# Kernel tuning notes

Measured on AMD Instinct MI355X. Metric: run time of the kernel, lower is better.

Reference implementation:

```python
import jax, jax.numpy as jnp
import numpy as np

# dims
B, L, V, E, H = 8, 2048, 32000, 512, 512
NUM_LAYERS, D_STATE, EXPAND, HEADDIM, D_CONV = 4, 64, 2, 64, 4
D_INNER = EXPAND * H                      # 1024
N_HEADS = D_INNER // HEADDIM              # 16
CONV_DIM = D_INNER + 2 * D_STATE          # 1152
D_PROJ = 2 * D_INNER + 2 * D_STATE + N_HEADS  # 2192 (z, xBC, dt)
PAD_IDX = 0
EPS = 1e-5


def silu(x):
    return x * jax.nn.sigmoid(x)


def _flip_len(x, lengths):
    # length-aware flip: reverse only the first `length` positions per sample
    t = jnp.arange(x.shape[1])[None, :]                 # (1, L)
    Lm = lengths[:, None]                               # (B, 1)
    idx = jnp.where(t < Lm, Lm - 1 - t, t)              # (B, L)
    return jnp.take_along_axis(x, idx[:, :, None], axis=1)


def _mamba2(x, W_in, conv_w, conv_b, dt_bias, A_log, Dp, norm_w, W_out):
    # Mamba2 forward (mamba_ssm semantics): in_proj -> causal depthwise conv ->
    # selective scan (SSD recurrence) -> gated RMSNorm -> out_proj.
    b, l, _ = x.shape
    zxbcdt = x @ W_in.T                                  # (b, l, D_PROJ)
    z, xBC, dt = jnp.split(zxbcdt, [D_INNER, D_INNER + CONV_DIM], axis=-1)
    # causal depthwise conv over time, kernel D_CONV
    xBC = jnp.transpose(xBC, (0, 2, 1))                  # (b, CONV_DIM, l)
    xBC = jax.lax.conv_general_dilated(
        xBC, conv_w[:, None, :], (1,), [(D_CONV - 1, 0)],
        feature_group_count=CONV_DIM)
    xBC = silu(xBC + conv_b[None, :, None])
    xBC = jnp.transpose(xBC, (0, 2, 1))                  # (b, l, CONV_DIM)
    xh, Bm, Cm = jnp.split(xBC, [D_INNER, D_INNER + D_STATE], axis=-1)
    dt = jax.nn.softplus(dt + dt_bias)                   # (b, l, nh)
    dA = jnp.exp(dt * (-jnp.exp(A_log)))                 # (b, l, nh)
    xh = xh.reshape(b, l, N_HEADS, HEADDIM)

    def step(s, inp):
        x_t, B_t, C_t, dA_t, dt_t = inp
        # s: (b, nh, hd, ds)
        s = s * dA_t[:, :, None, None] + (dt_t[:, :, None] * x_t)[..., None] * B_t[:, None, None, :]
        y = jnp.einsum('bnps,bs->bnp', s, C_t) + Dp[None, :, None] * x_t
        return s, y

    xs = (xh.transpose(1, 0, 2, 3), Bm.transpose(1, 0, 2), Cm.transpose(1, 0, 2),
          dA.transpose(1, 0, 2), dt.transpose(1, 0, 2))
    s0 = jnp.zeros((b, N_HEADS, HEADDIM, D_STATE), x.dtype)
    _, ys = jax.lax.scan(step, s0, xs)
    y = ys.transpose(1, 0, 2, 3).reshape(b, l, D_INNER)
    # gated RMSNorm then out projection
    y = y * silu(z)
    y = y * jax.lax.rsqrt(jnp.mean(y * y, axis=-1, keepdims=True) + EPS) * norm_w
    return y @ W_out.T


def _layernorm(x, g, b):
    mu = jnp.mean(x, axis=-1, keepdims=True)
    xc = x - mu
    var = jnp.mean(xc * xc, axis=-1, keepdims=True)
    return xc * jax.lax.rsqrt(var + EPS) * g + b


def setup_inputs() -> dict:
    key = jax.random.key(0)
    ks = iter(jax.random.split(key, 32))
    def nrm(shape, scale=0.02):
        return jax.random.normal(next(ks), shape, jnp.float32) * scale
    input_tokens = jax.random.randint(next(ks), (B, L), 1, V)
    src_lengths = jax.random.randint(next(ks), (B,), L // 2, L + 1)
    emb = nrm((V, E)).at[PAD_IDX].set(0.0)
    W_inp, b_inp = nrm((H, E)), jnp.zeros((H,), jnp.float32)
    m_Win = nrm((NUM_LAYERS, 2, D_PROJ, H))
    m_convw = nrm((NUM_LAYERS, 2, CONV_DIM, D_CONV), 0.2)
    m_convb = jnp.zeros((NUM_LAYERS, 2, CONV_DIM), jnp.float32)
    m_dtb = nrm((NUM_LAYERS, 2, N_HEADS), 0.5)
    m_Alog = jnp.log(jax.random.uniform(next(ks), (NUM_LAYERS, 2, N_HEADS), minval=1.0, maxval=16.0))
    m_D = jnp.ones((NUM_LAYERS, 2, N_HEADS), jnp.float32)
    m_norm = jnp.ones((NUM_LAYERS, 2, D_INNER), jnp.float32)
    m_Wout = nrm((NUM_LAYERS, 2, H, D_INNER))
    blk_Wo = nrm((NUM_LAYERS, H, 2 * H))
    blk_bo = jnp.zeros((NUM_LAYERS, H), jnp.float32)
    ln_g = jnp.ones((NUM_LAYERS, H), jnp.float32)
    ln_b = jnp.zeros((NUM_LAYERS, H), jnp.float32)
    W_enc, b_enc = nrm((2 * H, H)), jnp.zeros((2 * H,), jnp.float32)
    W_ad, b_ad = nrm((H, 2 * H)), jnp.zeros((H,), jnp.float32)
    return dict(input_tokens=input_tokens, src_lengths=src_lengths, emb=emb,
                W_inp=W_inp, b_inp=b_inp, m_Win=m_Win, m_convw=m_convw,
                m_convb=m_convb, m_dtb=m_dtb, m_Alog=m_Alog, m_D=m_D,
                m_norm=m_norm, m_Wout=m_Wout, blk_Wo=blk_Wo, blk_bo=blk_bo,
                ln_g=ln_g, ln_b=ln_b, W_enc=W_enc, b_enc=b_enc, W_ad=W_ad, b_ad=b_ad)


def reference(input_tokens, src_lengths, emb, W_inp, b_inp, m_Win, m_convw,
              m_convb, m_dtb, m_Alog, m_D, m_norm, m_Wout, blk_Wo, blk_bo,
              ln_g, ln_b, W_enc, b_enc, W_ad, b_ad):
    h = emb[input_tokens] @ W_inp.T + b_inp              # (B, L, H)
    for i in range(NUM_LAYERS):
        fwd = _mamba2(h, m_Win[i, 0], m_convw[i, 0], m_convb[i, 0], m_dtb[i, 0],
                      m_Alog[i, 0], m_D[i, 0], m_norm[i, 0], m_Wout[i, 0])
        hf = _flip_len(h, src_lengths)
        bwd = _mamba2(hf, m_Win[i, 1], m_convw[i, 1], m_convb[i, 1], m_dtb[i, 1],
                      m_Alog[i, 1], m_D[i, 1], m_norm[i, 1], m_Wout[i, 1])
        bwd = _flip_len(bwd, src_lengths)
        comb = jnp.concatenate([fwd, bwd], axis=-1)      # (B, L, 2H)
        out = comb @ blk_Wo[i].T + blk_bo[i]
        h = _layernorm(out + h, ln_g[i], ln_b[i])
    encoder_outputs = h @ W_enc.T + b_enc                # (B, L, 2H)
    mask = (jnp.arange(L)[None, :] < src_lengths[:, None]).astype(h.dtype)[..., None]
    denom = jnp.clip(src_lengths.astype(h.dtype), 1.0)[:, None]
    pooled = jnp.sum(encoder_outputs * mask, axis=1) / denom
    encoder_hidden = jnp.tanh(pooled @ W_ad.T + b_ad)[None]   # (1, B, H)
    return encoder_outputs, encoder_hidden
```

## Files before the change

### kernel.cpp

```cpp
#include <hip/hip_runtime.h>
#include <hip/hip_bf16.h>
#include <math.h>

using bf16 = __hip_bfloat16;
typedef __bf16 bf16x8 __attribute__((ext_vector_type(8)));
typedef float f32x4 __attribute__((ext_vector_type(4)));

#define B2F(x) __bfloat162float(x)
#define F2B(x) __float2bfloat16(x)

__device__ inline short f2bs(float x) { bf16 b = F2B(x); return *(short*)&b; }
__device__ inline float bs2f(short x) { bf16 b; *(short*)&b = x; return B2F(b); }

static constexpr int D_PROJ = 2192, CONV_DIM = 1152;
static constexpr int NCHUNK = 8, CLEN = 256;

static constexpr size_t OFF_H    = 0;
static constexpr size_t OFF_ZX   = 16777216;
static constexpr size_t OFF_XC   = 88604672;
static constexpr size_t OFF_S    = 126353408;
static constexpr size_t OFF_PT   = 143130624;
static constexpr size_t OFF_PC   = 144179200;
static constexpr size_t OFF_DTV  = 144183296;
static constexpr size_t OFF_DAV  = 145231872;
static constexpr size_t OFF_GIDX = 146280448;
static constexpr size_t OFF_POOL = 146345984;
static constexpr size_t OFF_WBF   = 146378752;
static constexpr size_t WBF_WIN   = 0;
static constexpr size_t WBF_WOUT  = 17956864;
static constexpr size_t WBF_BLK   = 26345472;
static constexpr size_t WBF_ENC   = 30539776;
static constexpr size_t WBF_BYTES = 31588352;

__global__ void k_wcvt(const float* __restrict__ src, bf16* __restrict__ dst, long n8)
{
    long i = (long)blockIdx.x * 256 + threadIdx.x;
    if (i >= n8) return;
    const float4* s = (const float4*)(src + i * 8);
    float4 f0 = s[0], f1 = s[1];
    short o[8];
    o[0] = f2bs(f0.x); o[1] = f2bs(f0.y); o[2] = f2bs(f0.z); o[3] = f2bs(f0.w);
    o[4] = f2bs(f1.x); o[5] = f2bs(f1.y); o[6] = f2bs(f1.z); o[7] = f2bs(f1.w);
    *(int4*)&dst[i * 8] = *(int4*)o;
}

__device__ inline void gl_lds16(const void* g, void* l)
{
    __builtin_amdgcn_global_load_lds(
        (const __attribute__((address_space(1))) unsigned int*)g,
        (__attribute__((address_space(3))) unsigned int*)l,
        16, 0, 0);
}

template<bool CF32>
__global__ __launch_bounds__(256, 2)
void k_gemm_bf(const bf16* __restrict__ A, const int* __restrict__ gatherIdx,
               const bf16* __restrict__ Wb, const float* __restrict__ bias,
               void* __restrict__ Cp, int M, int N, int K, int ldc, int coff)
{
    __shared__ union UU {
        struct { __align__(16) short As[128 * 64]; __align__(16) short Bs[128 * 64]; } ab;
        __align__(16) short Cs2[128 * 136];
        __align__(16) float Cs4[CF32 ? 128 * 132 : 4];
    } u;

    const int tid  = threadIdx.x;
    const int m0   = blockIdx.y * 128;
    const int n0   = blockIdx.x * 128;
    const int wave = tid >> 6, lane = tid & 63;
    const int l15  = lane & 15, quad = lane >> 4;
    const int wm   = (wave & 1) * 64, wn = (wave >> 1) * 64;

    const int sr   = lane >> 3;
    const int slot = lane & 7;
    const bf16* asrc[4];
    const bf16* bsrc[4];
    int ldsoff[4];
#pragma unroll
    for (int t = 0; t < 4; ++t) {
        int row = wave * 32 + t * 8 + sr;
        long arow = m0 + row;
        if (gatherIdx) arow = gatherIdx[m0 + row];
        int sl = ((slot ^ (row & 7)) * 8);
        asrc[t] = A + arow * (long)K + sl;
        int wr = n0 + row; if (wr > N - 1) wr = N - 1;
        bsrc[t] = Wb + (long)wr * K + sl;
        ldsoff[t] = (wave * 32 + t * 8) * 64;
    }

    int aoff[2][4], boff[2][4];
#pragma unroll
    for (int ks = 0; ks < 2; ++ks) {
        int swz = (((ks << 2) | quad) ^ (l15 & 7)) * 8;
#pragma unroll
        for (int i = 0; i < 4; ++i) {
            aoff[ks][i] = (wm + i * 16 + l15) * 64 + swz;
            boff[ks][i] = (wn + i * 16 + l15) * 64 + swz;
        }
    }

    f32x4 acc[4][4];
#pragma unroll
    for (int i = 0; i < 4; ++i)
#pragma unroll
        for (int j = 0; j < 4; ++j) acc[i][j] = f32x4{0.f, 0.f, 0.f, 0.f};

    for (int k0 = 0; k0 < K; k0 += 64) {
#pragma unroll
        for (int t = 0; t < 4; ++t) gl_lds16(asrc[t] + k0, &u.ab.As[ldsoff[t]]);
#pragma unroll
        for (int t = 0; t < 4; ++t) gl_lds16(bsrc[t] + k0, &u.ab.Bs[ldsoff[t]]);
        __syncthreads();

        bf16x8 af[2][4], bfr[2][4];
#pragma unroll
        for (int ks = 0; ks < 2; ++ks)
#pragma unroll
            for (int i = 0; i < 4; ++i) {
                af[ks][i]  = *(const bf16x8*)&u.ab.As[aoff[ks][i]];
                bfr[ks][i] = *(const bf16x8*)&u.ab.Bs[boff[ks][i]];
            }
#pragma unroll
        for (int ks = 0; ks < 2; ++ks)
#pragma unroll
            for (int i = 0; i < 4; ++i)
#pragma unroll
                for (int j = 0; j < 4; ++j)
                    acc[i][j] = __builtin_amdgcn_mfma_f32_16x16x32_bf16(af[ks][i], bfr[ks][j], acc[i][j], 0, 0, 0);
        __syncthreads();
    }

    __syncthreads();
    if (!CF32) {
#pragma unroll
        for (int j = 0; j < 4; ++j) {
            int lcol = wn + j * 16 + l15;
            int gcol = n0 + lcol;
            float bvv = (bias && gcol < N) ? bias[gcol] : 0.f;
#pragma unroll
            for (int i = 0; i < 4; ++i)
#pragma unroll
                for (int r = 0; r < 4; ++r)
                    u.Cs2[(wm + i * 16 + quad * 4 + r) * 136 + lcol] = f2bs(acc[i][j][r] + bvv);
        }
        __syncthreads();
        for (int i2 = tid; i2 < 2048; i2 += 256) {
            int lrow = i2 >> 4, seg = i2 & 15;
            int col0 = n0 + seg * 8;
            if (col0 < N) {
                int4 v = *(int4*)&u.Cs2[lrow * 136 + seg * 8];
                *(int4*)&((bf16*)Cp)[(long)(m0 + lrow) * ldc + coff + col0] = v;
            }
        }
    } else {
#pragma unroll
        for (int j = 0; j < 4; ++j) {
            int lcol = wn + j * 16 + l15;
            int gcol = n0 + lcol;
            float bvv = (bias && gcol < N) ? bias[gcol] : 0.f;
#pragma unroll
            for (int i = 0; i < 4; ++i)
#pragma unroll
                for (int r = 0; r < 4; ++r)
                    u.Cs4[(wm + i * 16 + quad * 4 + r) * 132 + lcol] = acc[i][j][r] + bvv;
        }
        __syncthreads();
        for (int i2 = tid; i2 < 4096; i2 += 256) {
            int lrow = i2 >> 5, seg = i2 & 31;
            int col0 = n0 + seg * 4;
            if (col0 < N) {
                int4 v = *(int4*)&u.Cs4[lrow * 132 + seg * 4];
                *(int4*)&((float*)Cp)[(long)(m0 + lrow) * ldc + coff + col0] = v;
            }
        }
    }
}

template<bool AF32, bool CF32>
__global__ __launch_bounds__(256, 2)
void k_gemm(const void* __restrict__ Ap, const int* __restrict__ gatherIdx,
            const float* __restrict__ W, const float* __restrict__ bias,
            void* __restrict__ Cp, int M, int N, int K, int ldc, int coff)
{
    __shared__ union UU {
        struct { __align__(16) short As[128 * 40]; __align__(16) short Bs[128 * 40]; } ab;
        __align__(16) short Cs2[128 * 136];
        __align__(16) float Cs4[CF32 ? 128 * 132 : 4];
    } u;

    const int tid  = threadIdx.x;
    const int m0   = blockIdx.y * 128;
    const int n0   = blockIdx.x * 128;
    const int wave = tid >> 6, lane = tid & 63;
    const int l15  = lane & 15, quad = lane >> 4;
    const int wm   = (wave & 1) * 64, wn = (wave >> 1) * 64;

    f32x4 acc[4][4];
#pragma unroll
    for (int i = 0; i < 4; ++i)
#pragma unroll
        for (int j = 0; j < 4; ++j) acc[i][j] = f32x4{0.f, 0.f, 0.f, 0.f};

    const int srow = tid >> 2;
    const int scol = (tid & 3) * 8;

    union V8 { int4 i4; short s[8]; };

    for (int k0 = 0; k0 < K; k0 += 32) {
        V8 av[2], bv[2];
#pragma unroll
        for (int it = 0; it < 2; ++it) {
            int r = srow + it * 64;
            long arow = m0 + r;
            if (gatherIdx) arow = gatherIdx[m0 + r];
            if (AF32) {
                const float* ap = (const float*)Ap + arow * (long)K + k0 + scol;
                float4 f0 = *(const float4*)ap;
                float4 f1 = *(const float4*)(ap + 4);
                av[it].s[0] = f2bs(f0.x); av[it].s[1] = f2bs(f0.y);
                av[it].s[2] = f2bs(f0.z); av[it].s[3] = f2bs(f0.w);
                av[it].s[4] = f2bs(f1.x); av[it].s[5] = f2bs(f1.y);
                av[it].s[6] = f2bs(f1.z); av[it].s[7] = f2bs(f1.w);
            } else {
                av[it].i4 = *(const int4*)((const bf16*)Ap + arow * (long)K + k0 + scol);
            }
            int wr = n0 + r;
            if (wr < N) {
                const float* wp = W + (long)wr * K + k0 + scol;
                float4 f0 = *(const float4*)wp;
                float4 f1 = *(const float4*)(wp + 4);
                bv[it].s[0] = f2bs(f0.x); bv[it].s[1] = f2bs(f0.y);
                bv[it].s[2] = f2bs(f0.z); bv[it].s[3] = f2bs(f0.w);
                bv[it].s[4] = f2bs(f1.x); bv[it].s[5] = f2bs(f1.y);
                bv[it].s[6] = f2bs(f1.z); bv[it].s[7] = f2bs(f1.w);
            } else {
                bv[it].i4 = int4{0, 0, 0, 0};
            }
        }
        __syncthreads();
#pragma unroll
        for (int it = 0; it < 2; ++it) {
            int r = srow + it * 64;
            *(int4*)&u.ab.As[r * 40 + scol] = av[it].i4;
            *(int4*)&u.ab.Bs[r * 40 + scol] = bv[it].i4;
        }
        __syncthreads();

        bf16x8 af[4], bfr[4];
#pragma unroll
        for (int i = 0; i < 4; ++i)
            af[i] = *(const bf16x8*)&u.ab.As[(wm + i * 16 + l15) * 40 + quad * 8];
#pragma unroll
        for (int j = 0; j < 4; ++j)
            bfr[j] = *(const bf16x8*)&u.ab.Bs[(wn + j * 16 + l15) * 40 + quad * 8];
#pragma unroll
        for (int i = 0; i < 4; ++i)
#pragma unroll
            for (int j = 0; j < 4; ++j)
                acc[i][j] = __builtin_amdgcn_mfma_f32_16x16x32_bf16(af[i], bfr[j], acc[i][j], 0, 0, 0);
    }

    __syncthreads();
    if (!CF32) {
#pragma unroll
        for (int j = 0; j < 4; ++j) {
            int lcol = wn + j * 16 + l15;
            int gcol = n0 + lcol;
            float bvv = (bias && gcol < N) ? bias[gcol] : 0.f;
#pragma unroll
            for (int i = 0; i < 4; ++i)
#pragma unroll
                for (int r = 0; r < 4; ++r)
                    u.Cs2[(wm + i * 16 + quad * 4 + r) * 136 + lcol] = f2bs(acc[i][j][r] + bvv);
        }
        __syncthreads();
        for (int i2 = tid; i2 < 2048; i2 += 256) {
            int lrow = i2 >> 4, seg = i2 & 15;
            int col0 = n0 + seg * 8;
            if (col0 < N) {
                int4 v = *(int4*)&u.Cs2[lrow * 136 + seg * 8];
                *(int4*)&((bf16*)Cp)[(long)(m0 + lrow) * ldc + coff + col0] = v;
            }
        }
    } else {
#pragma unroll
        for (int j = 0; j < 4; ++j) {
            int lcol = wn + j * 16 + l15;
            int gcol = n0 + lcol;
            float bvv = (bias && gcol < N) ? bias[gcol] : 0.f;
#pragma unroll
            for (int i = 0; i < 4; ++i)
#pragma unroll
                for (int r = 0; r < 4; ++r)
                    u.Cs4[(wm + i * 16 + quad * 4 + r) * 132 + lcol] = acc[i][j][r] + bvv;
        }
        __syncthreads();
        for (int i2 = tid; i2 < 4096; i2 += 256) {
            int lrow = i2 >> 5, seg = i2 & 31;
            int col0 = n0 + seg * 4;
            if (col0 < N) {
                int4 v = *(int4*)&u.Cs4[lrow * 132 + seg * 4];
                *(int4*)&((float*)Cp)[(long)(m0 + lrow) * ldc + coff + col0] = v;
            }
        }
    }
}

__global__ void k_mkidx(const int* __restrict__ lens, int* __restrict__ gidx)
{
    int idx = blockIdx.x * 256 + threadIdx.x;
    int b = idx >> 11, t = idx & 2047;
    int len = lens[b];
    gidx[idx] = b * 2048 + ((t < len) ? (len - 1 - t) : t);
}

__global__ __launch_bounds__(256)
void k_conv(const bf16* __restrict__ zx, const float* __restrict__ w,
            const float* __restrict__ cb, bf16* __restrict__ xc)
{
    const int bid = blockIdx.x;
    const int mb  = bid % 9;
    const int seg = bid / 9;
    const int b   = seg >> 3, tch = seg & 7;
    const int c0  = (mb * 16 + (threadIdx.x & 15)) * 8;
    const int trow = threadIdx.x >> 4;

    float wr[4][8], cbr[8];
#pragma unroll
    for (int i = 0; i < 8; i += 4) {
        float4 cv = *(const float4*)&cb[c0 + i];
        cbr[i] = cv.x; cbr[i+1] = cv.y; cbr[i+2] = cv.z; cbr[i+3] = cv.w;
    }
#pragma unroll
    for (int i = 0; i < 8; ++i) {
        float4 wv = *(const float4*)&w[(c0 + i) * 4];
        wr[0][i] = wv.x; wr[1][i] = wv.y; wr[2][i] = wv.z; wr[3][i] = wv.w;
    }

    const long base = (long)b * 2048 + tch * 256;
    for (int it = 0; it < 16; ++it) {
        const int t = it * 16 + trow;
        const long bt = base + t;
        const int tseq = tch * 256 + t;
        float acc[8];
#pragma unroll
        for (int i = 0; i < 8; ++i) acc[i] = cbr[i];
#pragma unroll
        for (int j = 0; j < 4; ++j) {
            if (tseq >= 3 - j) {
                bf16x8 v = *(const bf16x8*)&zx[(bt - 3 + j) * (long)D_PROJ + 1024 + c0];
#pragma unroll
                for (int i = 0; i < 8; ++i) acc[i] += wr[j][i] * (float)v[i];
            }
        }
        short out[8];
#pragma unroll
        for (int i = 0; i < 8; ++i) {
            float a = acc[i];
            out[i] = f2bs(a / (1.f + expf(-a)));
        }
        *(int4*)&xc[bt * (long)CONV_DIM + c0] = *(int4*)out;
    }
}

__global__ void k_dt(const bf16* __restrict__ zx, const float* __restrict__ dtb,
                     float* __restrict__ dtv)
{
    int idx = blockIdx.x * 256 + threadIdx.x;
    int hh = idx & 15;
    long bt = idx >> 4;
    float x  = B2F(zx[bt * (long)D_PROJ + 2176 + hh]) + dtb[hh];
    dtv[idx] = (x > 20.f) ? x : log1pf(expf(x));
}

__global__ __launch_bounds__(256, 2)
void k_ph1(const bf16* __restrict__ xc, const float* __restrict__ dtv,
           const float* __restrict__ alog, const float* __restrict__ Dp,
           bf16* __restrict__ y, float* __restrict__ Sl, float* __restrict__ Pc)
{
    const int blk = blockIdx.x;
    const int c = blk & 7, h = (blk >> 3) & 15, b = blk >> 7;
    const float Dv   = Dp[h];
    const float aexp = expf(alog[h]);

    __shared__ __align__(16) short B_s [64][72];
    __shared__ __align__(16) short C_s [64][72];
    __shared__ __align__(16) short XT  [64][72];
    __shared__ __align__(16) short BTw [64][72];
    __shared__ __align__(16) short P_s [64][72];
    __shared__ __align__(16) short hi_s[64][72];
    __shared__ __align__(16) short lo_s[64][72];
    __shared__ float cs_s[64];
    __shared__ float dt_l[64];

    const int tid  = threadIdx.x;
    const int wave = tid >> 6, lane = tid & 63;
    const int l15  = lane & 15, quad = lane >> 4;
    const int rr   = tid >> 3;
    const int sg8  = (tid & 7) * 8;

    const long base = (long)b * 2048;
    const int  tcs  = c * CLEN;
    float PcAcc = 1.f;

    for (int sc = 0; sc < 4; ++sc) {
        const int t0 = tcs + sc * 64;

#pragma unroll
        for (int it = 0; it < 2; ++it) {
            int r = rr + it * 32;
            const bf16* row = &xc[(base + t0 + r) * (long)CONV_DIM];
            bf16x8 xv = *(const bf16x8*)&row[h * 64 + sg8];
            *(int4*)&B_s[r][sg8] = *(const int4*)&row[1024 + sg8];
            *(int4*)&C_s[r][sg8] = *(const int4*)&row[1088 + sg8];
#pragma unroll
            for (int j = 0; j < 8; ++j) XT[sg8 + j][r] = ((short*)&xv)[j];
        }
        if (tid < 64) dt_l[tid] = dtv[((base + t0 + tid) << 4) + h];
        __syncthreads();

        if (wave == 0) {
            float d = dt_l[lane];
#pragma unroll
            for (int off = 1; off < 64; off <<= 1) {
                float u = __shfl_up(d, off);
                if (lane >= off) d += u;
            }
            cs_s[lane] = d;
        }
        __syncthreads();

        {
            float cs63 = cs_s[63];
#pragma unroll
            for (int it = 0; it < 2; ++it) {
                int s = rr + it * 32;
                float ws = expf(aexp * (cs_s[s] - cs63)) * dt_l[s];
                bf16x8 bv = *(const bf16x8*)&B_s[s][sg8];
#pragma unroll
                for (int j = 0; j < 8; ++j) BTw[sg8 + j][s] = f2bs((float)bv[j] * ws);
            }
        }
        __syncthreads();

        float pD[4][4];
        {
            const int sb = wave * 16;
            f32x4 acc[4];
#pragma unroll
            for (int tt = 0; tt < 4; ++tt) acc[tt] = f32x4{0.f, 0.f, 0.f, 0.f};
#pragma unroll
            for (int kst = 0; kst < 2; ++kst) {
                bf16x8 aB = *(const bf16x8*)&B_s[sb + l15][kst * 32 + quad * 8];
#pragma unroll
                for (int tt = 0; tt < 4; ++tt) {
                    bf16x8 wC = *(const bf16x8*)&C_s[tt * 16 + l15][kst * 32 + quad * 8];
                    acc[tt] = __builtin_amdgcn_mfma_f32_16x16x32_bf16(aB, wC, acc[tt], 0, 0, 0);
                }
            }
            float csS[4], dtS[4];
            int sIdx[4];
#pragma unroll
            for (int r = 0; r < 4; ++r) {
                sIdx[r] = sb + quad * 4 + r;
                csS[r] = cs_s[sIdx[r]];
                dtS[r] = dt_l[sIdx[r]];
            }
#pragma unroll
            for (int tt = 0; tt < 4; ++tt) {
                int t = tt * 16 + l15;
                float csT = cs_s[t];
#pragma unroll
                for (int r = 0; r < 4; ++r) {
                    float m = (sIdx[r] <= t) ? expf(aexp * (csS[r] - csT)) * dtS[r] : 0.f;
                    pD[tt][r] = acc[tt][r] * m;
                }
            }
        }
        __syncthreads();
        {
            const int sb = wave * 16;
#pragma unroll
            for (int tt = 0; tt < 4; ++tt) {
                int t = tt * 16 + l15;
#pragma unroll
                for (int r = 0; r < 4; ++r) {
                    int s = sb + quad * 4 + r;
                    short hb = f2bs(pD[tt][r]);
                    P_s[t][s] = hb;
                    B_s[t][s] = f2bs(pD[tt][r] - bs2f(hb));
                }
            }
        }
        __syncthreads();

        {
            const int tb = wave * 16;
            f32x4 acc[4];
#pragma unroll
            for (int pp = 0; pp < 4; ++pp) acc[pp] = f32x4{0.f, 0.f, 0.f, 0.f};
            if (sc > 0) {
#pragma unroll
                for (int kst = 0; kst < 2; ++kst) {
                    bf16x8 aC = *(const bf16x8*)&C_s[tb + l15][kst * 32 + quad * 8];
#pragma unroll
                    for (int pp = 0; pp < 4; ++pp) {
                        bf16x8 wH = *(const bf16x8*)&hi_s[pp * 16 + l15][kst * 32 + quad * 8];
                        acc[pp] = __builtin_amdgcn_mfma_f32_16x16x32_bf16(aC, wH, acc[pp], 0, 0, 0);
                        bf16x8 wL = *(const bf16x8*)&lo_s[pp * 16 + l15][kst * 32 + quad * 8];
                        acc[pp] = __builtin_amdgcn_mfma_f32_16x16x32_bf16(aC, wL, acc[pp], 0, 0, 0);
                    }
                }
#pragma unroll
                for (int r = 0; r < 4; ++r) {
                    float g = expf(-aexp * cs_s[tb + quad * 4 + r]);
#pragma unroll
                    for (int pp = 0; pp < 4; ++pp) acc[pp][r] *= g;
                }
            }
#pragma unroll
            for (int kst = 0; kst < 2; ++kst) {
                bf16x8 aPh = *(const bf16x8*)&P_s[tb + l15][kst * 32 + quad * 8];
                bf16x8 aPl = *(const bf16x8*)&B_s[tb + l15][kst * 32 + quad * 8];
#pragma unroll
                for (int pp = 0; pp < 4; ++pp) {
                    bf16x8 wX = *(const bf16x8*)&XT[pp * 16 + l15][kst * 32 + quad * 8];
                    acc[pp] = __builtin_amdgcn_mfma_f32_16x16x32_bf16(aPh, wX, acc[pp], 0, 0, 0);
                    acc[pp] = __builtin_amdgcn_mfma_f32_16x16x32_bf16(aPl, wX, acc[pp], 0, 0, 0);
                }
            }
#pragma unroll
            for (int pp = 0; pp < 4; ++pp) {
#pragma unroll
                for (int r = 0; r < 4; ++r) {
                    int t = tb + quad * 4 + r, p = pp * 16 + l15;
                    float xv = bs2f(XT[p][t]);
                    P_s[t][p] = f2bs(acc[pp][r] + Dv * xv);
                }
            }
        }
        __syncthreads();

#pragma unroll
        for (int it = 0; it < 2; ++it) {
            int r = rr + it * 32;
            *(int4*)&y[(base + t0 + r) * 1024L + h * 64 + sg8] = *(int4*)&P_s[r][sg8];
        }
        {
            const int pb = wave * 16;
            f32x4 acc2[4];
#pragma unroll
            for (int nn = 0; nn < 4; ++nn) acc2[nn] = f32x4{0.f, 0.f, 0.f, 0.f};
#pragma unroll
            for (int kst = 0; kst < 2; ++kst) {
                bf16x8 aX = *(const bf16x8*)&XT[pb + l15][kst * 32 + quad * 8];
#pragma unroll
                for (int nn = 0; nn < 4; ++nn) {
                    bf16x8 wB = *(const bf16x8*)&BTw[nn * 16 + l15][kst * 32 + quad * 8];
                    acc2[nn] = __builtin_amdgcn_mfma_f32_16x16x32_bf16(aX, wB, acc2[nn], 0, 0, 0);
                }
            }
            float Pcv = expf(-aexp * cs_s[63]);
            PcAcc *= Pcv;
#pragma unroll
            for (int nn = 0; nn < 4; ++nn) {
#pragma unroll
                for (int r = 0; r < 4; ++r) {
                    int p = pb + quad * 4 + r, n = nn * 16 + l15;
                    float Sn = acc2[nn][r];
                    if (sc > 0) Sn += Pcv * (bs2f(hi_s[p][n]) + bs2f(lo_s[p][n]));
                    short hb = f2bs(Sn);
                    hi_s[p][n] = hb;
                    lo_s[p][n] = f2bs(Sn - bs2f(hb));
                }
            }
        }
        __syncthreads();
    }

    for (int i = tid; i < 4096; i += 256) {
        int p = i >> 6, n = i & 63;
        Sl[(long)blk * 4096 + i] = bs2f(hi_s[p][n]) + bs2f(lo_s[p][n]);
    }
    if (tid == 0) Pc[blk] = PcAcc;
}

__global__ __launch_bounds__(256)
void k_comb(float* __restrict__ Sl, const float* __restrict__ Pc)
{
    int bh = blockIdx.x;
    int tid = threadIdx.x;
    float run[16];
#pragma unroll
    for (int i = 0; i < 16; ++i) run[i] = 0.f;
    for (int c = 0; c < NCHUNK; ++c) {
        float* ptr = Sl + ((long)(bh * NCHUNK + c)) * 4096 + tid * 16;
        float pc = Pc[bh * NCHUNK + c];
#pragma unroll
        for (int q = 0; q < 4; ++q) {
            float4 v = *(float4*)&ptr[q * 4];
            float4 init = float4{run[q*4+0], run[q*4+1], run[q*4+2], run[q*4+3]};
            run[q*4+0] = v.x + pc * run[q*4+0];
            run[q*4+1] = v.y + pc * run[q*4+1];
            run[q*4+2] = v.z + pc * run[q*4+2];
            run[q*4+3] = v.w + pc * run[q*4+3];
            *(float4*)&ptr[q * 4] = init;
        }
    }
}

__global__ __launch_bounds__(256, 2)
void k_ph3(const float* __restrict__ Sl, const bf16* __restrict__ xc,
           const float* __restrict__ dtv, const float* __restrict__ alog,
           bf16* __restrict__ y)
{
    const int blk = blockIdx.x;
    const int c = blk & 7, h = (blk >> 3) & 15, b = blk >> 7;
    if (c == 0) return;
    const float aexp = expf(alog[h]);

    __shared__ __align__(16) short C_s [64][72];
    __shared__ __align__(16) short S_hi[64][72];
    __shared__ __align__(16) short S_lo[64][72];
    __shared__ __align__(16) short ysb [64][72];
    __shared__ float dt_l[64], cs_s[64];

    const int tid  = threadIdx.x;
    const int wave = tid >> 6, lane = tid & 63;
    const int l15  = lane & 15, quad = lane >> 4;
    const int rr   = tid >> 3, sg8 = (tid & 7) * 8;

    const long base = (long)b * 2048;
    const int  tcs  = c * CLEN;

    for (int i = tid; i < 4096; i += 256) {
        int p = i >> 6, n = i & 63;
        float v = Sl[(long)blk * 4096 + i];
        short hb = f2bs(v);
        S_hi[p][n] = hb;
        S_lo[p][n] = f2bs(v - bs2f(hb));
    }

    float csoff = 0.f;
    for (int tile = 0; tile < 4; ++tile) {
        const int t0 = tcs + tile * 64;
#pragma unroll
        for (int it = 0; it < 2; ++it) {
            int r = rr + it * 32;
            *(int4*)&C_s[r][sg8] =
                *(const int4*)&xc[(base + t0 + r) * (long)CONV_DIM + 1088 + sg8];
        }
        if (tid < 64) dt_l[tid] = dtv[((base + t0 + tid) << 4) + h];
        __syncthreads();

        if (wave == 0) {
            float d = dt_l[lane];
#pragma unroll
            for (int off = 1; off < 64; off <<= 1) {
                float u = __shfl_up(d, off);
                if (lane >= off) d += u;
            }
            cs_s[lane] = d;
        }
        __syncthreads();

        {
            const int tb = wave * 16;
            f32x4 acc[4];
#pragma unroll
            for (int pp = 0; pp < 4; ++pp) acc[pp] = f32x4{0.f, 0.f, 0.f, 0.f};
#pragma unroll
            for (int kst = 0; kst < 2; ++kst) {
                bf16x8 aC = *(const bf16x8*)&C_s[tb + l15][kst * 32 + quad * 8];
#pragma unroll
                for (int pp = 0; pp < 4; ++pp) {
                    bf16x8 wH = *(const bf16x8*)&S_hi[pp * 16 + l15][kst * 32 + quad * 8];
                    acc[pp] = __builtin_amdgcn_mfma_f32_16x16x32_bf16(aC, wH, acc[pp], 0, 0, 0);
                    bf16x8 wL = *(const bf16x8*)&S_lo[pp * 16 + l15][kst * 32 + quad * 8];
                    acc[pp] = __builtin_amdgcn_mfma_f32_16x16x32_bf16(aC, wL, acc[pp], 0, 0, 0);
                }
            }
#pragma unroll
            for (int r = 0; r < 4; ++r) {
                int t = tb + quad * 4 + r;
                float pt = expf(-aexp * (csoff + cs_s[t]));
#pragma unroll
                for (int pp = 0; pp < 4; ++pp)
                    ysb[t][pp * 16 + l15] = f2bs(acc[pp][r] * pt);
            }
        }
        __syncthreads();

        for (int i = tid; i < 512; i += 256) {
            int r = i >> 3, cc = (i & 7) * 8;
            bf16* yp = &y[(base + t0 + r) * 1024L + h * 64 + cc];
            int4 ov = *(int4*)yp;
            short* os = (short*)&ov;
            short nv[8];
#pragma unroll
            for (int j = 0; j < 8; ++j)
                nv[j] = f2bs(bs2f(os[j]) + bs2f(ysb[r][cc + j]));
            *(int4*)yp = *(int4*)nv;
        }
        csoff += cs_s[63];
        __syncthreads();
    }
}

__global__ __launch_bounds__(256)
void k_gate(bf16* __restrict__ yp, const bf16* __restrict__ zxp,
            const float* __restrict__ nw)
{
    long bt = blockIdx.x;
    bf16* y = yp + bt * 1024;
    const bf16* z = zxp + bt * (long)D_PROJ;
    int tid = threadIdx.x;
    ushort4 zv = *(const ushort4*)&z[tid * 4];
    ushort4 yv = *(const ushort4*)&y[tid * 4];
    float g[4], ss = 0.f;
    {
        float zz0 = bs2f((short)zv.x), zz1 = bs2f((short)zv.y);
        float zz2 = bs2f((short)zv.z), zz3 = bs2f((short)zv.w);
        float yy0 = bs2f((short)yv.x), yy1 = bs2f((short)yv.y);
        float yy2 = bs2f((short)yv.z), yy3 = bs2f((short)yv.w);
        g[0] = yy0 * (zz0 / (1.f + expf(-zz0)));
        g[1] = yy1 * (zz1 / (1.f + expf(-zz1)));
        g[2] = yy2 * (zz2 / (1.f + expf(-zz2)));
        g[3] = yy3 * (zz3 / (1.f + expf(-zz3)));
        ss = g[0]*g[0] + g[1]*g[1] + g[2]*g[2] + g[3]*g[3];
    }
#pragma unroll
    for (int o = 1; o < 64; o <<= 1) ss += __shfl_xor(ss, o);
    __shared__ float red[4];
    if ((tid & 63) == 0) red[tid >> 6] = ss;
    __syncthreads();
    float tot = red[0] + red[1] + red[2] + red[3];
    float sc = rsqrtf(tot * (1.f / 1024.f) + 1e-5f);
    const float* w = nw + tid * 4;
    ushort4 ov;
    ov.x = (unsigned short)f2bs(g[0] * sc * w[0]);
    ov.y = (unsigned short)f2bs(g[1] * sc * w[1]);
    ov.z = (unsigned short)f2bs(g[2] * sc * w[2]);
    ov.w = (unsigned short)f2bs(g[3] * sc * w[3]);
    *(ushort4*)&y[tid * 4] = ov;
}

__global__ void k_swap(bf16* __restrict__ buf, const int* __restrict__ lens)
{
    int idx = blockIdx.x * 256 + threadIdx.x;
    int v = idx & 127;
    int r = idx >> 7;
    int b = r >> 10, t = r & 1023;
    int len = lens[b];
    int t2 = len - 1 - t;
    if (t < len && t < t2) {
        int4* p = (int4*)buf;
        long i1 = ((long)b * 2048 + t)  * 128 + v;
        long i2 = ((long)b * 2048 + t2) * 128 + v;
        int4 a = p[i1], c = p[i2];
        p[i1] = c; p[i2] = a;
    }
}

__global__ __launch_bounds__(256)
void k_ln(const bf16* __restrict__ outb, bf16* __restrict__ h,
          const float* __restrict__ g, const float* __restrict__ bb)
{
    long r = (long)blockIdx.x * 512;
    int tid = threadIdx.x;
    float v0 = B2F(outb[r + tid])       + B2F(h[r + tid]);
    float v1 = B2F(outb[r + tid + 256]) + B2F(h[r + tid + 256]);
    __shared__ float red[4], red2[4];
    float s = v0 + v1;
#pragma unroll
    for (int o = 1; o < 64; o <<= 1) s += __shfl_xor(s, o);
    if ((tid & 63) == 0) red[tid >> 6] = s;
    __syncthreads();
    float mu = (red[0] + red[1] + red[2] + red[3]) * (1.f / 512.f);
    float d0 = v0 - mu, d1 = v1 - mu;
    float q = d0 * d0 + d1 * d1;
#pragma unroll
    for (int o = 1; o < 64; o <<= 1) q += __shfl_xor(q, o);
    if ((tid & 63) == 0) red2[tid >> 6] = q;
    __syncthreads();
    float var = (red2[0] + red2[1] + red2[2] + red2[3]) * (1.f / 512.f);
    float rs = rsqrtf(var + 1e-5f);
    h[r + tid]       = F2B(d0 * rs * g[tid]       + bb[tid]);
    h[r + tid + 256] = F2B(d1 * rs * g[tid + 256] + bb[tid + 256]);
}

__global__ void k_pool(const float* __restrict__ enc, const int* __restrict__ lens,
                       float* __restrict__ pooled)
{
    int bid = blockIdx.x;
    int b = bid >> 6;
    int cg = (bid >> 4) & 3, tc = bid & 15;
    int c = cg * 256 + threadIdx.x;
    int len = lens[b];
    float s = 0.f;
    int tend = tc * 128 + 128;
    for (int t = tc * 128; t < tend; ++t)
        if (t < len) s += enc[((long)b * 2048 + t) * 1024 + c];
    atomicAdd(&pooled[b * 1024 + c], s);
}

__global__ void k_adapter(const float* __restrict__ pooled, const float* __restrict__ Wad,
                          const float* __restrict__ bad, const int* __restrict__ lens,
                          float* __restrict__ outh)
{
    int idx = blockIdx.x * 256 + threadIdx.x;
    int b = idx >> 9, j = idx & 511;
    const float* wrow = Wad + (long)j * 1024;
    const float* prow = pooled + b * 1024;
    float acc = 0.f;
    for (int k = 0; k < 1024; ++k) acc += prow[k] * wrow[k];
    int li = lens[b]; if (li < 1) li = 1;
    acc = acc / (float)li + bad[j];
    outh[idx] = tanhf(acc);
}

static void gemm(const void* A, bool af32, const int* gather, const float* W,
                 const float* bias, void* C, bool cf32,
                 int M, int N, int K, int ldc, int coff, hipStream_t s)
{
    dim3 grid((N + 127) / 128, M / 128);
    if (af32) {
        if (cf32) k_gemm<true,  true ><<<grid, 256, 0, s>>>(A, gather, W, bias, C, M, N, K, ldc, coff);
        else      k_gemm<true,  false><<<grid, 256, 0, s>>>(A, gather, W, bias, C, M, N, K, ldc, coff);
    } else {
        if (cf32) k_gemm<false, true ><<<grid, 256, 0, s>>>(A, gather, W, bias, C, M, N, K, ldc, coff);
        else      k_gemm<false, false><<<grid, 256, 0, s>>>(A, gather, W, bias, C, M, N, K, ldc, coff);
    }
}

static void gemm_bf(const bf16* A, const int* gather, const bf16* Wb, const float* bias,
                    void* C, bool cf32, int M, int N, int K, int ldc, int coff, hipStream_t s)
{
    dim3 grid((N + 127) / 128, M / 128);
    if (cf32) k_gemm_bf<true ><<<grid, 256, 0, s>>>(A, gather, Wb, bias, C, M, N, K, ldc, coff);
    else      k_gemm_bf<false><<<grid, 256, 0, s>>>(A, gather, Wb, bias, C, M, N, K, ldc, coff);
}

extern "C" void kernel_launch(void* const* d_in, const int* in_sizes, int n_in,
                              void* d_out, int out_size, void* d_ws, size_t ws_size,
                              hipStream_t stream)
{
    const int*   tok    = (const int*)d_in[0];
    const int*   lens   = (const int*)d_in[1];
    const float* emb    = (const float*)d_in[2];
    const float* W_inp  = (const float*)d_in[3];
    const float* b_inp  = (const float*)d_in[4];
    const float* m_Win  = (const float*)d_in[5];
    const float* m_convw= (const float*)d_in[6];
    const float* m_convb= (const float*)d_in[7];
    const float* m_dtb  = (const float*)d_in[8];
    const float* m_Alog = (const float*)d_in[9];
    const float* m_D    = (const float*)d_in[10];
    const float* m_norm = (const float*)d_in[11];
    const float* m_Wout = (const float*)d_in[12];
    const float* blk_Wo = (const float*)d_in[13];
    const float* blk_bo = (const float*)d_in[14];
    const float* ln_g   = (const float*)d_in[15];
    const float* ln_b   = (const float*)d_in[16];
    const float* W_enc  = (const float*)d_in[17];
    const float* b_enc  = (const float*)d_in[18];
    const float* W_ad   = (const float*)d_in[19];
    const float* b_ad   = (const float*)d_in[20];

    char* ws = (char*)d_ws;
    bf16*  h      = (bf16*)(ws + OFF_H);
    bf16*  zx     = (bf16*)(ws + OFF_ZX);
    bf16*  xc     = (bf16*)(ws + OFF_XC);
    float* Sl     = (float*)(ws + OFF_S);
    float* Pc     = (float*)(ws + OFF_PC);
    float* dtv    = (float*)(ws + OFF_DTV);
    int*   gidx   = (int*)(ws + OFF_GIDX);
    float* pooled = (float*)(ws + OFF_POOL);

    float* dout   = (float*)d_out;
    bf16*  y_f    = (bf16*)d_out;
    bf16*  y_b    = (bf16*)d_out + (size_t)16384 * 1024;
    bf16*  comb   = (bf16*)(ws + OFF_ZX);
    bf16*  outbuf = (bf16*)(ws + OFF_XC);

    const bool fast = ws_size >= (size_t)(OFF_WBF + WBF_BYTES);
    bf16* wWin  = fast ? (bf16*)(ws + OFF_WBF + WBF_WIN)  : nullptr;
    bf16* wWout = fast ? (bf16*)(ws + OFF_WBF + WBF_WOUT) : nullptr;
    bf16* wBlk  = fast ? (bf16*)(ws + OFF_WBF + WBF_BLK)  : nullptr;
    bf16* wEnc  = fast ? (bf16*)(ws + OFF_WBF + WBF_ENC)  : nullptr;
    if (fast) {
        k_wcvt<<<(1122304 + 255) / 256, 256, 0, stream>>>(m_Win,  wWin,  1122304);
        k_wcvt<<<( 524288 + 255) / 256, 256, 0, stream>>>(m_Wout, wWout,  524288);
        k_wcvt<<<( 262144 + 255) / 256, 256, 0, stream>>>(blk_Wo, wBlk,   262144);
        k_wcvt<<<(  65536 + 255) / 256, 256, 0, stream>>>(W_enc,  wEnc,    65536);
    }

    k_mkidx<<<64, 256, 0, stream>>>(lens, gidx);

    gemm(emb, true, tok, W_inp, b_inp, h, false, 16384, 512, 512, 512, 0, stream);

    for (int l = 0; l < 4; ++l) {
        for (int dir = 0; dir < 2; ++dir) {
            const float* Wi = m_Win  + (size_t)(l * 2 + dir) * D_PROJ * 512;
            const float* cw = m_convw + (size_t)(l * 2 + dir) * CONV_DIM * 4;
            const float* cbp= m_convb + (size_t)(l * 2 + dir) * CONV_DIM;
            const float* dtb= m_dtb  + l * 32 + dir * 16;
            const float* alg= m_Alog + l * 32 + dir * 16;
            const float* Dpp= m_D    + l * 32 + dir * 16;
            const float* nw = m_norm + (size_t)(l * 2 + dir) * 1024;
            bf16* y = dir ? y_b : y_f;

            if (fast)
                gemm_bf(h, dir ? gidx : nullptr, wWin + (size_t)(l * 2 + dir) * D_PROJ * 512,
                        nullptr, zx, false, 16384, D_PROJ, 512, D_PROJ, 0, stream);
            else
                gemm(h, false, dir ? gidx : nullptr, Wi, nullptr, zx, false,
                     16384, D_PROJ, 512, D_PROJ, 0, stream);
            k_conv<<<576, 256, 0, stream>>>(zx, cw, cbp, xc);
            k_dt<<<1024, 256, 0, stream>>>(zx, dtb, dtv);
            k_ph1<<<1024, 256, 0, stream>>>(xc, dtv, alg, Dpp, y, Sl, Pc);
            k_comb<<<128, 256, 0, stream>>>(Sl, Pc);
            k_ph3<<<1024, 256, 0, stream>>>(Sl, xc, dtv, alg, y);
            k_gate<<<16384, 256, 0, stream>>>(y, zx, nw);
            if (dir) k_swap<<<4096, 256, 0, stream>>>(y_b, lens);
        }

        if (fast) {
            gemm_bf(y_f, nullptr, wWout + (size_t)(l * 2 + 0) * 512 * 1024, nullptr, comb,
                    false, 16384, 512, 1024, 1024, 0, stream);
            gemm_bf(y_b, nullptr, wWout + (size_t)(l * 2 + 1) * 512 * 1024, nullptr, comb,
                    false, 16384, 512, 1024, 1024, 512, stream);
            gemm_bf(comb, nullptr, wBlk + (size_t)l * 512 * 1024, blk_bo + l * 512, outbuf,
                    false, 16384, 512, 1024, 512, 0, stream);
        } else {
            gemm(y_f, false, nullptr, m_Wout + (size_t)(l * 2 + 0) * 512 * 1024, nullptr, comb,
                 false, 16384, 512, 1024, 1024, 0, stream);
            gemm(y_b, false, nullptr, m_Wout + (size_t)(l * 2 + 1) * 512 * 1024, nullptr, comb,
                 false, 16384, 512, 1024, 1024, 512, stream);
            gemm(comb, false, nullptr, blk_Wo + (size_t)l * 512 * 1024, blk_bo + l * 512, outbuf,
                 false, 16384, 512, 1024, 512, 0, stream);
        }
        k_ln<<<16384, 256, 0, stream>>>(outbuf, h, ln_g + l * 512, ln_b + l * 512);
    }

    if (fast)
        gemm_bf(h, nullptr, wEnc, b_enc, dout, true, 16384, 1024, 512, 1024, 0, stream);
    else
        gemm(h, false, nullptr, W_enc, b_enc, dout, true, 16384, 1024, 512, 1024, 0, stream);

    hipMemsetAsync(pooled, 0, 8 * 1024 * sizeof(float), stream);
    k_pool<<<512, 256, 0, stream>>>(dout, lens, pooled);
    k_adapter<<<16, 256, 0, stream>>>(pooled, W_ad, b_ad, lens, dout + (size_t)16384 * 1024);
}
```

Before: 2.470 ms.

## Pre-transpose x and B for the SSD chunk kernel and move the D-skip into the gate

Adds a k_xt kernel that writes x (per head) and B into time-major transposed global buffers. This lets the rewritten chunk-scan kernel load its operands directly into XOR-swizzled LDS instead of transposing them element by element. The new k_ph1 folds the decay weights into B before the state MFMA and uses swizzled LDS throughout. The D*x skip term moves into the gating kernel, and the bf16 GEMM launch bounds are raised to 4 blocks per CU. In exchange this costs an extra transpose pass, extra workspace, and possible register pressure in the GEMM, and the new path only runs when the workspace is large enough.

New measurement: 2.366 ms. 4.2% less time.

```diff
diff --git a/kernel.cpp b/kernel.cpp
--- a/kernel.cpp
+++ b/kernel.cpp
@@ -19,10 +19,8 @@
 static constexpr size_t OFF_ZX   = 16777216;
 static constexpr size_t OFF_XC   = 88604672;
 static constexpr size_t OFF_S    = 126353408;
-static constexpr size_t OFF_PT   = 143130624;
 static constexpr size_t OFF_PC   = 144179200;
 static constexpr size_t OFF_DTV  = 144183296;
-static constexpr size_t OFF_DAV  = 145231872;
 static constexpr size_t OFF_GIDX = 146280448;
 static constexpr size_t OFF_POOL = 146345984;
 static constexpr size_t OFF_WBF   = 146378752;
@@ -31,6 +29,12 @@
 static constexpr size_t WBF_BLK   = 26345472;
 static constexpr size_t WBF_ENC   = 30539776;
 static constexpr size_t WBF_BYTES = 31588352;
+static constexpr size_t OFF_XT    = 177967104;
+static constexpr size_t OFF_BT    = 211521536;
+static constexpr size_t WS_NEED2  = 213618688;
+
+__device__ __forceinline__ int swz16(int r, int g) { return r * 64 + ((g ^ (r & 7)) << 3); }
+__device__ __forceinline__ int swz1(int r, int c) { return r * 64 + ((((c) >> 3) ^ (r & 7)) << 3) + (c & 7); }
 
 __global__ void k_wcvt(const float* __restrict__ src, bf16* __restrict__ dst, long n8)
 {
@@ -53,7 +57,7 @@
 }
 
 template<bool CF32>
-__global__ __launch_bounds__(256, 2)
+__global__ __launch_bounds__(256, 4)
 void k_gemm_bf(const bf16* __restrict__ A, const int* __restrict__ gatherIdx,
                const bf16* __restrict__ Wb, const float* __restrict__ bias,
                void* __restrict__ Cp, int M, int N, int K, int ldc, int coff)
@@ -373,10 +377,261 @@
     dtv[idx] = (x > 20.f) ? x : log1pf(expf(x));
 }
 
+__global__ __launch_bounds__(256)
+void k_xt(const bf16* __restrict__ xc, bf16* __restrict__ xtg, bf16* __restrict__ btg)
+{
+    __shared__ short T[64 * 66];
+    const int bid  = blockIdx.x;
+    const int g    = bid % 17;
+    const int rest = bid / 17;
+    const int tile = rest & 31;
+    const int b    = rest >> 5;
+    const int tid  = threadIdx.x;
+    const int src0 = (g < 16) ? g * 64 : 1024;
+    const long rowbase = (long)b * 2048 + tile * 64;
+
+#pragma unroll
+    for (int it = 0; it < 2; ++it) {
+        int r  = (tid >> 3) + it * 32;
+        int cg = (tid & 7) * 8;
+        int4 v = *(const int4*)&xc[(rowbase + r) * (long)CONV_DIM + src0 + cg];
+        const int* vi = (const int*)&v;
+#pragma unroll
+        for (int m = 0; m < 4; ++m)
+            *(int*)&T[r * 66 + cg + 2 * m] = vi[m];
+    }
+    __syncthreads();
+#pragma unroll
+    for (int it = 0; it < 2; ++it) {
+        int ch = (tid >> 3) + it * 32;
+        int tg = (tid & 7) * 8;
+        short o[8];
+#pragma unroll
+        for (int k = 0; k < 8; ++k) o[k] = T[(tg + k) * 66 + ch];
+        bf16* dp;
+        if (g < 16) dp = &xtg[((long)((b * 16 + g) * 64 + ch) << 11) + tile * 64 + tg];
+        else        dp = &btg[((long)ch << 14) + (long)b * 2048 + tile * 64 + tg];
+        *(int4*)dp = *(int4*)o;
+    }
+}
+
+__global__ __launch_bounds__(256, 3)
+void k_ph1(const bf16* __restrict__ xc, const bf16* __restrict__ xt,
+           const bf16* __restrict__ btg, const float* __restrict__ dtv,
+           const float* __restrict__ alog,
+           bf16* __restrict__ y, float* __restrict__ Sl, float* __restrict__ Pc)
+{
+    const int blk = blockIdx.x;
+    const int c = blk & 7, h = (blk >> 3) & 15, b = blk >> 7;
+    const float aexp = expf(alog[h]);
+
+    __shared__ __align__(16) short B_s [4096];
+    __shared__ __align__(16) short C_s [4096];
+    __shared__ __align__(16) short XT_ [4096];
+    __shared__ __align__(16) short PB  [4096];
+    __shared__ __align__(16) short hi_s[4096];
+    __shared__ __align__(16) short lo_s[4096];
+    __shared__ float cs_s[64], dt_l[64], ws_s[64];
+
+    const int tid  = threadIdx.x;
+    const int wave = tid >> 6, lane = tid & 63;
+    const int l15  = lane & 15, quad = lane >> 4;
+    const int rr   = tid >> 3, g8 = tid & 7;
+
+    const long base = (long)b * 2048;
+    const int  tcs  = c * CLEN;
+    const bf16* xtb = xt + ((long)(b * 16 + h) << 17);
+    float PcAcc = 1.f;
+
+    for (int sc = 0; sc < 4; ++sc) {
+        const int t0 = tcs + sc * 64;
+
+#pragma unroll
+        for (int it = 0; it < 2; ++it) {
+            int r = rr + it * 32;
+            const bf16* row = &xc[(base + t0 + r) * (long)CONV_DIM];
+            *(int4*)&B_s[swz16(r, g8)] = *(const int4*)&row[1024 + g8 * 8];
+            *(int4*)&C_s[swz16(r, g8)] = *(const int4*)&row[1088 + g8 * 8];
+            *(int4*)&XT_[swz16(r, g8)] = *(const int4*)&xtb[((long)r << 11) + t0 + g8 * 8];
+        }
+        if (tid < 64) dt_l[tid] = dtv[((base + t0 + tid) << 4) + h];
+        __syncthreads();
+
+        if (wave == 0) {
+            float d = dt_l[lane];
+#pragma unroll
+            for (int off = 1; off < 64; off <<= 1) {
+                float u = __shfl_up(d, off);
+                if (lane >= off) d += u;
+            }
+            cs_s[lane] = d;
+        }
+        __syncthreads();
+
+        if (tid < 64) ws_s[tid] = expf(aexp * (cs_s[tid] - cs_s[63])) * dt_l[tid];
+        __syncthreads();
+
+#pragma unroll
+        for (int it = 0; it < 2; ++it) {
+            int n = rr + it * 32;
+            bf16x8 bv = *(const bf16x8*)&btg[((long)n << 14) + base + t0 + g8 * 8];
+            short o[8];
+#pragma unroll
+            for (int j = 0; j < 8; ++j) o[j] = f2bs((float)bv[j] * ws_s[g8 * 8 + j]);
+            *(int4*)&PB[swz16(n, g8)] = *(int4*)o;
+        }
+        __syncthreads();
+
+        f32x4 sl4[4];
+        {
+            const int pb = wave * 16;
+#pragma unroll
+            for (int nn = 0; nn < 4; ++nn) sl4[nn] = f32x4{0.f, 0.f, 0.f, 0.f};
+#pragma unroll
+            for (int kst = 0; kst < 2; ++kst) {
+                bf16x8 aX = *(const bf16x8*)&XT_[swz16(pb + l15, kst * 4 + quad)];
+#pragma unroll
+                for (int nn = 0; nn < 4; ++nn) {
+                    bf16x8 wB = *(const bf16x8*)&PB[swz16(nn * 16 + l15, kst * 4 + quad)];
+                    sl4[nn] = __builtin_amdgcn_mfma_f32_16x16x32_bf16(aX, wB, sl4[nn], 0, 0, 0);
+                }
+            }
+        }
+        float pD[4][4];
+        {
+            const int sb = wave * 16;
+            f32x4 acc[4];
+#pragma unroll
+            for (int tt = 0; tt < 4; ++tt) acc[tt] = f32x4{0.f, 0.f, 0.f, 0.f};
+#pragma unroll
+            for (int kst = 0; kst < 2; ++kst) {
+                bf16x8 aB = *(const bf16x8*)&B_s[swz16(sb + l15, kst * 4 + quad)];
+#pragma unroll
+                for (int tt = 0; tt < 4; ++tt) {
+                    bf16x8 wC = *(const bf16x8*)&C_s[swz16(tt * 16 + l15, kst * 4 + quad)];
+                    acc[tt] = __builtin_amdgcn_mfma_f32_16x16x32_bf16(aB, wC, acc[tt], 0, 0, 0);
+                }
+            }
+            float csS[4], dtS[4];
+            int sIdx[4];
+#pragma unroll
+            for (int r = 0; r < 4; ++r) {
+                sIdx[r] = sb + quad * 4 + r;
+                csS[r] = cs_s[sIdx[r]];
+                dtS[r] = dt_l[sIdx[r]];
+            }
+#pragma unroll
+            for (int tt = 0; tt < 4; ++tt) {
+                int t = tt * 16 + l15;
+                float csT = cs_s[t];
+#pragma unroll
+                for (int r = 0; r < 4; ++r) {
+                    float m = (sIdx[r] <= t) ? expf(aexp * (csS[r] - csT)) * dtS[r] : 0.f;
+                    pD[tt][r] = acc[tt][r] * m;
+                }
+            }
+        }
+        __syncthreads();
+        {
+            const int sb = wave * 16;
+#pragma unroll
+            for (int tt = 0; tt < 4; ++tt) {
+                int t = tt * 16 + l15;
+#pragma unroll
+                for (int r = 0; r < 4; ++r) {
+                    int s = sb + quad * 4 + r;
+                    short hb = f2bs(pD[tt][r]);
+                    PB [swz1(t, s)] = hb;
+                    B_s[swz1(t, s)] = f2bs(pD[tt][r] - bs2f(hb));
+                }
+            }
+        }
+        __syncthreads();
+
+        {
+            const int tb = wave * 16;
+            f32x4 acc[4];
+#pragma unroll
+            for (int pp = 0; pp < 4; ++pp) acc[pp] = f32x4{0.f, 0.f, 0.f, 0.f};
+            if (sc > 0) {
+#pragma unroll
+                for (int kst = 0; kst < 2; ++kst) {
+                    bf16x8 aC = *(const bf16x8*)&C_s[swz16(tb + l15, kst * 4 + quad)];
+#pragma unroll
+                    for (int pp = 0; pp < 4; ++pp) {
+                        bf16x8 wH = *(const bf16x8*)&hi_s[swz16(pp * 16 + l15, kst * 4 + quad)];
+                        acc[pp] = __builtin_amdgcn_mfma_f32_16x16x32_bf16(aC, wH, acc[pp], 0, 0, 0);
+                        bf16x8 wL = *(const bf16x8*)&lo_s[swz16(pp * 16 + l15, kst * 4 + quad)];
+                        acc[pp] = __builtin_amdgcn_mfma_f32_16x16x32_bf16(aC, wL, acc[pp], 0, 0, 0);
+                    }
+                }
+#pragma unroll
+                for (int r = 0; r < 4; ++r) {
+                    float g = expf(-aexp * cs_s[tb + quad * 4 + r]);
+#pragma unroll
+                    for (int pp = 0; pp < 4; ++pp) acc[pp][r] *= g;
+                }
+            }
+#pragma unroll
+            for (int kst = 0; kst < 2; ++kst) {
+                bf16x8 aPh = *(const bf16x8*)&PB [swz16(tb + l15, kst * 4 + quad)];
+                bf16x8 aPl = *(const bf16x8*)&B_s[swz16(tb + l15, kst * 4 + quad)];
+#pragma unroll
+                for (int pp = 0; pp < 4; ++pp) {
+                    bf16x8 wX = *(const bf16x8*)&XT_[swz16(pp * 16 + l15, kst * 4 + quad)];
+                    acc[pp] = __builtin_amdgcn_mfma_f32_16x16x32_bf16(aPh, wX, acc[pp], 0, 0, 0);
+                    acc[pp] = __builtin_amdgcn_mfma_f32_16x16x32_bf16(aPl, wX, acc[pp], 0, 0, 0);
+                }
+            }
+#pragma unroll
+            for (int pp = 0; pp < 4; ++pp) {
+#pragma unroll
+                for (int r = 0; r < 4; ++r) {
+                    int t = tb + quad * 4 + r, p = pp * 16 + l15;
+                    PB[swz1(t, p)] = f2bs(acc[pp][r]);
+                }
+            }
+        }
+        __syncthreads();
+
+#pragma unroll
+        for (int it = 0; it < 2; ++it) {
+            int r = rr + it * 32;
+            *(int4*)&y[(base + t0 + r) * 1024L + h * 64 + g8 * 8] = *(int4*)&PB[swz16(r, g8)];
+        }
+        {
+            const int pb = wave * 16;
+            float Pcv = expf(-aexp * cs_s[63]);
+            PcAcc *= Pcv;
+#pragma unroll
+            for (int nn = 0; nn < 4; ++nn) {
+#pragma unroll
+                for (int r = 0; r < 4; ++r) {
+                    int p = pb + quad * 4 + r, n = nn * 16 + l15;
+                    int ix = swz1(p, n);
+                    float Sn = sl4[nn][r];
+                    if (sc > 0) Sn += Pcv * (bs2f(hi_s[ix]) + bs2f(lo_s[ix]));
+                    short hb = f2bs(Sn);
+                    hi_s[ix] = hb;
+                    lo_s[ix] = f2bs(Sn - bs2f(hb));
+                }
+            }
+        }
+    }
+
+    __syncthreads();
+    for (int i = tid; i < 4096; i += 256) {
+        int p = i >> 6, n = i & 63;
+        int ix = swz1(p, n);
+        Sl[(long)blk * 4096 + i] = bs2f(hi_s[ix]) + bs2f(lo_s[ix]);
+    }
+    if (tid == 0) Pc[blk] = PcAcc;
+}
+
 __global__ __launch_bounds__(256, 2)
-void k_ph1(const bf16* __restrict__ xc, const float* __restrict__ dtv,
-           const float* __restrict__ alog, const float* __restrict__ Dp,
-           bf16* __restrict__ y, float* __restrict__ Sl, float* __restrict__ Pc)
+void k_ph1_fb(const bf16* __restrict__ xc, const float* __restrict__ dtv,
+              const float* __restrict__ alog, const float* __restrict__ Dp,
+              bf16* __restrict__ y, float* __restrict__ Sl, float* __restrict__ Pc)
 {
     const int blk = blockIdx.x;
     const int c = blk & 7, h = (blk >> 3) & 15, b = blk >> 7;
@@ -405,7 +660,6 @@
 
     for (int sc = 0; sc < 4; ++sc) {
         const int t0 = tcs + sc * 64;
-
 #pragma unroll
         for (int it = 0; it < 2; ++it) {
             int r = rr + it * 32;
@@ -707,9 +961,11 @@
     }
 }
 
+template<bool ADDX>
 __global__ __launch_bounds__(256)
 void k_gate(bf16* __restrict__ yp, const bf16* __restrict__ zxp,
-            const float* __restrict__ nw)
+            const float* __restrict__ nw, const bf16* __restrict__ xcp,
+            const float* __restrict__ Dp)
 {
     long bt = blockIdx.x;
     bf16* y = yp + bt * 1024;
@@ -717,12 +973,21 @@
     int tid = threadIdx.x;
     ushort4 zv = *(const ushort4*)&z[tid * 4];
     ushort4 yv = *(const ushort4*)&y[tid * 4];
+    float dx[4] = {0.f, 0.f, 0.f, 0.f};
+    if (ADDX) {
+        float Dv = Dp[tid >> 4];
+        ushort4 xv = *(const ushort4*)&xcp[bt * (long)CONV_DIM + tid * 4];
+        dx[0] = Dv * bs2f((short)xv.x);
+        dx[1] = Dv * bs2f((short)xv.y);
+        dx[2] = Dv * bs2f((short)xv.z);
+        dx[3] = Dv * bs2f((short)xv.w);
+    }
     float g[4], ss = 0.f;
     {
         float zz0 = bs2f((short)zv.x), zz1 = bs2f((short)zv.y);
         float zz2 = bs2f((short)zv.z), zz3 = bs2f((short)zv.w);
-        float yy0 = bs2f((short)yv.x), yy1 = bs2f((short)yv.y);
-        float yy2 = bs2f((short)yv.z), yy3 = bs2f((short)yv.w);
+        float yy0 = bs2f((short)yv.x) + dx[0], yy1 = bs2f((short)yv.y) + dx[1];
+        float yy2 = bs2f((short)yv.z) + dx[2], yy3 = bs2f((short)yv.w) + dx[3];
         g[0] = yy0 * (zz0 / (1.f + expf(-zz0)));
         g[1] = yy1 * (zz1 / (1.f + expf(-zz1)));
         g[2] = yy2 * (zz2 / (1.f + expf(-zz2)));
@@ -883,11 +1148,14 @@
     bf16*  comb   = (bf16*)(ws + OFF_ZX);
     bf16*  outbuf = (bf16*)(ws + OFF_XC);
 
-    const bool fast = ws_size >= (size_t)(OFF_WBF + WBF_BYTES);
+    const bool fast  = ws_size >= (size_t)(OFF_WBF + WBF_BYTES);
+    const bool fast2 = fast && ws_size >= (size_t)WS_NEED2;
     bf16* wWin  = fast ? (bf16*)(ws + OFF_WBF + WBF_WIN)  : nullptr;
     bf16* wWout = fast ? (bf16*)(ws + OFF_WBF + WBF_WOUT) : nullptr;
     bf16* wBlk  = fast ? (bf16*)(ws + OFF_WBF + WBF_BLK)  : nullptr;
     bf16* wEnc  = fast ? (bf16*)(ws + OFF_WBF + WBF_ENC)  : nullptr;
+    bf16* xtg   = fast2 ? (bf16*)(ws + OFF_XT) : nullptr;
+    bf16* btg   = fast2 ? (bf16*)(ws + OFF_BT) : nullptr;
     if (fast) {
         k_wcvt<<<(1122304 + 255) / 256, 256, 0, stream>>>(m_Win,  wWin,  1122304);
         k_wcvt<<<( 524288 + 255) / 256, 256, 0, stream>>>(m_Wout, wWout,  524288);
@@ -918,10 +1186,16 @@
                      16384, D_PROJ, 512, D_PROJ, 0, stream);
             k_conv<<<576, 256, 0, stream>>>(zx, cw, cbp, xc);
             k_dt<<<1024, 256, 0, stream>>>(zx, dtb, dtv);
-            k_ph1<<<1024, 256, 0, stream>>>(xc, dtv, alg, Dpp, y, Sl, Pc);
+            if (fast2) {
+                k_xt<<<4352, 256, 0, stream>>>(xc, xtg, btg);
+                k_ph1<<<1024, 256, 0, stream>>>(xc, xtg, btg, dtv, alg, y, Sl, Pc);
+            } else {
+                k_ph1_fb<<<1024, 256, 0, stream>>>(xc, dtv, alg, Dpp, y, Sl, Pc);
+            }
             k_comb<<<128, 256, 0, stream>>>(Sl, Pc);
             k_ph3<<<1024, 256, 0, stream>>>(Sl, xc, dtv, alg, y);
-            k_gate<<<16384, 256, 0, stream>>>(y, zx, nw);
+            if (fast2) k_gate<true ><<<16384, 256, 0, stream>>>(y, zx, nw, xc, Dpp);
+            else       k_gate<false><<<16384, 256, 0, stream>>>(y, zx, nw, nullptr, nullptr);
             if (dir) k_swap<<<4096, 256, 0, stream>>>(y_b, lens);
         }
 
```
